# Kernel tuning notes

Hardware: AMD Instinct MI355X
Metric: run time of the kernel (lower is better)

## Reference

```python
import jax, jax.numpy as jnp
import numpy as np

B, IN, N, E = 2048, 1024, 64, 128
NEG_SLOPE = 0.01  # torch LeakyReLU default

def setup_inputs() -> dict:
    key = jax.random.key(0)
    k = jax.random.split(key, 5)
    scale_in = 1.0 / np.sqrt(IN)
    scale_ctx = 1.0 / np.sqrt(2 * E)
    return {
        "x": jax.random.normal(k[0], (B, IN), dtype=jnp.float32),
        # stacked per-concept Linear(in_features, 2*emb_size)
        "W_ctx": jax.random.uniform(k[1], (N, IN, 2 * E), jnp.float32, -scale_in, scale_in),
        "b_ctx": jax.random.uniform(k[2], (N, 2 * E), jnp.float32, -scale_in, scale_in),
        # shared Linear(2*emb_size, 1)
        "w_prob": jax.random.uniform(k[3], (2 * E,), jnp.float32, -scale_ctx, scale_ctx),
        "b_prob": jax.random.uniform(k[4], (), jnp.float32, -scale_ctx, scale_ctx),
    }

def reference(x, W_ctx, b_ctx, w_prob, b_prob):
    # context: [B, N, 2E] = LeakyReLU(x @ W_i + b_i) for all concepts i at once
    ctx = jnp.einsum("bi,nio->bno", x, W_ctx) + b_ctx
    ctx = jnp.where(ctx >= 0, ctx, NEG_SLOPE * ctx)
    # shared gate: [B, N]
    c_pred = jax.nn.sigmoid(jnp.einsum("bno,o->bn", ctx, w_prob) + b_prob)
    # gated blend of positive/negative halves -> [B, N, E]
    p = c_pred[..., None]
    c_emb = ctx[..., :E] * p + ctx[..., E:] * (1.0 - p)
    return c_emb, c_pred
```

## Files before the change

kernel.cpp:

```cpp
#include <hip/hip_runtime.h>
#include <hip/hip_bf16.h>

typedef __attribute__((ext_vector_type(4))) short short4v;
typedef __attribute__((ext_vector_type(8))) short short8v;
typedef __attribute__((ext_vector_type(4))) float floatx4;

#define B_ROWS 2048
#define K_DIM  1024
#define N_CON  64
#define TWO_E  256
#define E_DIM  128
#define BM     128
#define BK     64
#define NT     16
#define LDSA_BYTES (BM * BK * 2)
#define LDSB_BYTES (TWO_E * BK * 2)
#define TILE_BYTES (LDSA_BYTES + LDSB_BYTES)
#define NBUF 3
#define SMEM_DYN (TILE_BYTES * NBUF)
#define EMB_ELEMS 16777216ULL
#define WT_BYTES  33554432ULL
#define XB_BYTES  4194304ULL

static __device__ inline unsigned short bf16bits(float f) {
    __hip_bfloat16 h = __float2bfloat16(f);
    unsigned short u;
    __builtin_memcpy(&u, &h, 2);
    return u;
}

static __device__ inline void dma16(const void* g, void* l) {
    __builtin_amdgcn_global_load_lds(
        (const __attribute__((address_space(1))) unsigned int*)g,
        (__attribute__((address_space(3))) unsigned int*)l,
        16, 0, 0);
}

__global__ void __launch_bounds__(256) prep(const float* __restrict__ W,
                                            const float* __restrict__ x,
                                            unsigned short* __restrict__ Wt,
                                            unsigned short* __restrict__ xb) {
    __shared__ unsigned int lds2[64 * 36];
    const int tid = threadIdx.x;
    const int ot = blockIdx.x, ktile = blockIdx.y, n = blockIdx.z;
    const float* src = W + ((size_t)n * K_DIM + (size_t)ktile * 64) * TWO_E + ot * 64;
    unsigned short* dst = Wt + ((size_t)n * TWO_E + (size_t)ot * 64) * K_DIM + ktile * 64;

    const int kp = tid >> 4;
    const int c  = (tid & 15) * 4;
#pragma unroll
    for (int it = 0; it < 2; ++it) {
        const int k0 = it * 32 + kp * 2;
        floatx4 r0 = *(const floatx4*)&src[(size_t)k0 * TWO_E + c];
        floatx4 r1 = *(const floatx4*)&src[(size_t)(k0 + 1) * TWO_E + c];
#pragma unroll
        for (int j = 0; j < 4; ++j) {
            unsigned int d = (unsigned int)bf16bits(r0[j]) |
                             ((unsigned int)bf16bits(r1[j]) << 16);
            lds2[(c + j) * 36 + it * 16 + kp] = d;
        }
    }
    __syncthreads();
#pragma unroll
    for (int it = 0; it < 2; ++it) {
        int q = it * 256 + tid;
        int o = q >> 3, kc = q & 7;
        short8v v = *(short8v*)&lds2[o * 36 + kc * 4];
        *(short8v*)&dst[(size_t)o * K_DIM + kc * 8] = v;
    }

    const int bid = blockIdx.x + blockIdx.y * 4 + blockIdx.z * 64;
    const size_t base = (size_t)bid * 512 + (size_t)tid * 2;
    unsigned int d = (unsigned int)bf16bits(x[base]) |
                     ((unsigned int)bf16bits(x[base + 1]) << 16);
    ((unsigned int*)xb)[base >> 1] = d;
}

static __device__ inline void stage_A(const unsigned short* xrow, int kt,
                                      char* ldsA, int wave, int lane) {
#pragma unroll
    for (int it = 0; it < 2; ++it) {
        int c = it * 8 + wave;
        int s = c * 64 + lane;
        int r = s >> 3, g = s & 7;
        dma16(xrow + (size_t)r * K_DIM + kt + ((g ^ (r & 7)) * 8), ldsA + c * 1024);
    }
}

template <int I0, int I1>
static __device__ inline void stage_B(const unsigned short* wbase, int kt,
                                      char* ldsB, int wave, int lane) {
#pragma unroll
    for (int it = I0; it < I1; ++it) {
        int c = it * 8 + wave;
        int s = c * 64 + lane;
        int r = s >> 3, g = s & 7;
        dma16(wbase + (size_t)r * K_DIM + kt + ((g ^ (r & 7)) * 8), ldsB + c * 1024);
    }
}

__global__ void __launch_bounds__(512, 2)
concept_pipe(const unsigned short* __restrict__ xb,
             const unsigned short* __restrict__ Wt,
             const float* __restrict__ bc,
             const float* __restrict__ wp,
             const float* __restrict__ bp,
             float* __restrict__ out) {
    extern __shared__ __align__(16) char smem[];

    const int tid  = threadIdx.x;
    const int wave = tid >> 6;
    const int lane = tid & 63;
    const int lg   = lane >> 4;
    const int l15  = lane & 15;
    const int h    = wave >> 2;
    const int og   = wave & 3;

    const int lin = blockIdx.y * 16 + blockIdx.x;
    const int nid = (lin & 7) * 128 + (lin >> 3);
    const int rb  = nid & 15;
    const int n   = nid >> 4;

    int otile[4];
#pragma unroll
    for (int oi = 0; oi < 4; ++oi) otile[oi] = og * 32 + (oi & 1) * 16 + (oi & 2) * 64;

    floatx4 acc[4][4];
#pragma unroll
    for (int mi = 0; mi < 4; ++mi)
#pragma unroll
        for (int oi = 0; oi < 4; ++oi) acc[mi][oi] = (floatx4){0.f, 0.f, 0.f, 0.f};

    const unsigned short* xrow  = xb + (size_t)rb * BM * K_DIM;
    const unsigned short* wbase = Wt + (size_t)n * TWO_E * K_DIM;

    stage_A(xrow, 0, smem, wave, lane);
    stage_B<0, 4>(wbase, 0, smem + LDSA_BYTES, wave, lane);
    stage_A(xrow, BK, smem + TILE_BYTES, wave, lane);
    stage_B<0, 4>(wbase, BK, smem + TILE_BYTES + LDSA_BYTES, wave, lane);

    asm volatile("s_waitcnt vmcnt(6)" ::: "memory");
    __builtin_amdgcn_s_barrier();

    int cur = 0;
#pragma unroll 1
    for (int t = 0; t < NT; ++t) {
        char* ldsA = smem + cur * TILE_BYTES;
        char* ldsB = ldsA + LDSA_BYTES;
        int stg = cur + 2; if (stg >= NBUF) stg -= NBUF;
        char* stgA = smem + stg * TILE_BYTES;
        char* stgB = stgA + LDSA_BYTES;
        const int ktn = (t + 2) * BK;

        short8v af[4], bfr[4];

        {
            const int sw = (lg ^ (l15 & 7)) * 16;
#pragma unroll
            for (int mi = 0; mi < 4; ++mi)
                af[mi] = *(const short8v*)(ldsA + (h * 64 + mi * 16 + l15) * 128 + sw);
#pragma unroll
            for (int oi = 0; oi < 4; ++oi)
                bfr[oi] = *(const short8v*)(ldsB + (otile[oi] + l15) * 128 + sw);
        }
        if (t <= NT - 3) {
            stage_A(xrow, ktn, stgA, wave, lane);
            stage_B<0, 1>(wbase, ktn, stgB, wave, lane);
        }
        __builtin_amdgcn_s_barrier();
        asm volatile("s_waitcnt lgkmcnt(0)" ::: "memory");
        __builtin_amdgcn_sched_barrier(0);
        __builtin_amdgcn_s_setprio(1);
#pragma unroll
        for (int mi = 0; mi < 4; ++mi)
#pragma unroll
            for (int oi = 0; oi < 4; ++oi)
                acc[mi][oi] = __builtin_amdgcn_mfma_f32_16x16x32_bf16(
                    af[mi], bfr[oi], acc[mi][oi], 0, 0, 0);
        __builtin_amdgcn_s_setprio(0);
        __builtin_amdgcn_s_barrier();

        {
            const int sw = ((4 + lg) ^ (l15 & 7)) * 16;
#pragma unroll
            for (int mi = 0; mi < 4; ++mi)
                af[mi] = *(const short8v*)(ldsA + (h * 64 + mi * 16 + l15) * 128 + sw);
#pragma unroll
            for (int oi = 0; oi < 4; ++oi)
                bfr[oi] = *(const short8v*)(ldsB + (otile[oi] + l15) * 128 + sw);
        }
        if (t <= NT - 3)
            stage_B<1, 4>(wbase, ktn, stgB, wave, lane);
        __builtin_amdgcn_s_barrier();
        asm volatile("s_waitcnt lgkmcnt(0)" ::: "memory");
        __builtin_amdgcn_sched_barrier(0);
        __builtin_amdgcn_s_setprio(1);
#pragma unroll
        for (int mi = 0; mi < 4; ++mi)
#pragma unroll
            for (int oi = 0; oi < 4; ++oi)
                acc[mi][oi] = __builtin_amdgcn_mfma_f32_16x16x32_bf16(
                    af[mi], bfr[oi], acc[mi][oi], 0, 0, 0);
        __builtin_amdgcn_s_setprio(0);

        if (t <= NT - 3)      asm volatile("s_waitcnt vmcnt(6)" ::: "memory");
        else if (t == NT - 2) asm volatile("s_waitcnt vmcnt(0)" ::: "memory");
        if (t < NT - 1) __builtin_amdgcn_s_barrier();

        ++cur; if (cur == NBUF) cur = 0;
    }

    __syncthreads();

    float biasf[4], wpf[4];
#pragma unroll
    for (int oi = 0; oi < 4; ++oi) {
        int o = otile[oi] + l15;
        biasf[oi] = bc[n * TWO_E + o];
        wpf[oi]  = wp[o];
    }
#pragma unroll
    for (int mi = 0; mi < 4; ++mi)
#pragma unroll
        for (int oi = 0; oi < 4; ++oi)
#pragma unroll
            for (int j = 0; j < 4; ++j) {
                float v = acc[mi][oi][j] + biasf[oi];
                acc[mi][oi][j] = v >= 0.f ? v : 0.01f * v;
            }

    float* partial = (float*)smem;
    float* pv      = (float*)(smem + 2048);

#pragma unroll
    for (int mi = 0; mi < 4; ++mi)
#pragma unroll
        for (int j = 0; j < 4; ++j) {
            float ps = 0.f;
#pragma unroll
            for (int oi = 0; oi < 4; ++oi) ps += acc[mi][oi][j] * wpf[oi];
            ps += __shfl_xor(ps, 1);
            ps += __shfl_xor(ps, 2);
            ps += __shfl_xor(ps, 4);
            ps += __shfl_xor(ps, 8);
            if (l15 == 0) partial[(h * 64 + mi * 16 + lg * 4 + j) * 4 + og] = ps;
        }
    __syncthreads();

    if (tid < 128) {
        float s = partial[tid * 4] + partial[tid * 4 + 1] + partial[tid * 4 + 2] +
                  partial[tid * 4 + 3] + bp[0];
        float p = 1.f / (1.f + __expf(-s));
        pv[tid] = p;
        size_t bi = (size_t)rb * BM + tid;
        out[EMB_ELEMS + bi * N_CON + n] = p;
    }
    __syncthreads();

#pragma unroll
    for (int mi = 0; mi < 4; ++mi)
#pragma unroll
        for (int oi = 0; oi < 2; ++oi)
#pragma unroll
            for (int j = 0; j < 4; ++j) {
                int row = h * 64 + mi * 16 + lg * 4 + j;
                int e = og * 32 + oi * 16 + l15;
                float p = pv[row];
                float v = acc[mi][oi][j] * p + acc[mi][oi + 2][j] * (1.f - p);
                size_t bi = (size_t)rb * BM + row;
                out[(bi * N_CON + n) * E_DIM + e] = v;
            }
}

__global__ void __launch_bounds__(512, 4)
concept_fallback(const float* __restrict__ x,
                 const float* __restrict__ Wc,
                 const float* __restrict__ bc,
                 const float* __restrict__ wp,
                 const float* __restrict__ bp,
                 float* __restrict__ out) {
    __shared__ __align__(16) char smem[TILE_BYTES];
    char* ldsA = smem;
    char* ldsB = smem + LDSA_BYTES;

    const int tid  = threadIdx.x;
    const int wave = tid >> 6;
    const int lane = tid & 63;
    const int lg   = lane >> 4;
    const int l15  = lane & 15;
    const int h    = wave >> 2;
    const int og   = wave & 3;
    const int rb = blockIdx.x;
    const int n  = blockIdx.y;

    int otile[4];
#pragma unroll
    for (int oi = 0; oi < 4; ++oi) otile[oi] = og * 32 + (oi & 1) * 16 + (oi & 2) * 64;

    floatx4 acc[4][4];
#pragma unroll
    for (int mi = 0; mi < 4; ++mi)
#pragma unroll
        for (int oi = 0; oi < 4; ++oi) acc[mi][oi] = (floatx4){0.f, 0.f, 0.f, 0.f};

    const float* xg = x + (size_t)rb * BM * K_DIM;
    const float* wg = Wc + (size_t)n * K_DIM * TWO_E;

    for (int kt = 0; kt < K_DIM; kt += BK) {
#pragma unroll
        for (int it = 0; it < 2; ++it) {
            int s = it * 512 + tid;
            int r = s >> 3, g = s & 7;
            const float* p = xg + (size_t)r * K_DIM + kt + ((g ^ (r & 7)) * 8);
            floatx4 v0 = *(const floatx4*)p, v1 = *(const floatx4*)(p + 4);
            short8v b;
            b[0] = (short)bf16bits(v0[0]); b[1] = (short)bf16bits(v0[1]);
            b[2] = (short)bf16bits(v0[2]); b[3] = (short)bf16bits(v0[3]);
            b[4] = (short)bf16bits(v1[0]); b[5] = (short)bf16bits(v1[1]);
            b[6] = (short)bf16bits(v1[2]); b[7] = (short)bf16bits(v1[3]);
            *(short8v*)(ldsA + s * 16) = b;
        }
#pragma unroll
        for (int it = 0; it < 4; ++it) {
            int s = it * 512 + tid;
            int r = s >> 3, g = s & 7;
            int k0 = kt + (g ^ (r & 7)) * 8;
            short8v b;
#pragma unroll
            for (int j = 0; j < 8; ++j)
                b[j] = (short)bf16bits(wg[(size_t)(k0 + j) * TWO_E + r]);
            *(short8v*)(ldsB + s * 16) = b;
        }
        __syncthreads();

#pragma unroll
        for (int ks = 0; ks < 2; ++ks) {
            const int sw = ((ks * 4 + lg) ^ (l15 & 7)) * 16;
            short8v af[4], bfr[4];
#pragma unroll
            for (int mi = 0; mi < 4; ++mi)
                af[mi] = *(const short8v*)(ldsA + (h * 64 + mi * 16 + l15) * 128 + sw);
#pragma unroll
            for (int oi = 0; oi < 4; ++oi)
                bfr[oi] = *(const short8v*)(ldsB + (otile[oi] + l15) * 128 + sw);
#pragma unroll
            for (int mi = 0; mi < 4; ++mi)
#pragma unroll
                for (int oi = 0; oi < 4; ++oi)
                    acc[mi][oi] = __builtin_amdgcn_mfma_f32_16x16x32_bf16(
                        af[mi], bfr[oi], acc[mi][oi], 0, 0, 0);
        }
        __syncthreads();
    }

    float biasf[4], wpf[4];
#pragma unroll
    for (int oi = 0; oi < 4; ++oi) {
        int o = otile[oi] + l15;
        biasf[oi] = bc[n * TWO_E + o];
        wpf[oi]  = wp[o];
    }
#pragma unroll
    for (int mi = 0; mi < 4; ++mi)
#pragma unroll
        for (int oi = 0; oi < 4; ++oi)
#pragma unroll
            for (int j = 0; j < 4; ++j) {
                float v = acc[mi][oi][j] + biasf[oi];
                acc[mi][oi][j] = v >= 0.f ? v : 0.01f * v;
            }

    float* partial = (float*)smem;
    float* pv      = (float*)(smem + 2048);

#pragma unroll
    for (int mi = 0; mi < 4; ++mi)
#pragma unroll
        for (int j = 0; j < 4; ++j) {
            float ps = 0.f;
#pragma unroll
            for (int oi = 0; oi < 4; ++oi) ps += acc[mi][oi][j] * wpf[oi];
            ps += __shfl_xor(ps, 1);
            ps += __shfl_xor(ps, 2);
            ps += __shfl_xor(ps, 4);
            ps += __shfl_xor(ps, 8);
            if (l15 == 0) partial[(h * 64 + mi * 16 + lg * 4 + j) * 4 + og] = ps;
        }
    __syncthreads();

    if (tid < 128) {
        float s = partial[tid * 4] + partial[tid * 4 + 1] + partial[tid * 4 + 2] +
                  partial[tid * 4 + 3] + bp[0];
        float p = 1.f / (1.f + __expf(-s));
        pv[tid] = p;
        size_t bi = (size_t)rb * BM + tid;
        out[EMB_ELEMS + bi * N_CON + n] = p;
    }
    __syncthreads();

#pragma unroll
    for (int mi = 0; mi < 4; ++mi)
#pragma unroll
        for (int oi = 0; oi < 2; ++oi)
#pragma unroll
            for (int j = 0; j < 4; ++j) {
                int row = h * 64 + mi * 16 + lg * 4 + j;
                int e = og * 32 + oi * 16 + l15;
                float p = pv[row];
                float v = acc[mi][oi][j] * p + acc[mi][oi + 2][j] * (1.f - p);
                size_t bi = (size_t)rb * BM + row;
                out[(bi * N_CON + n) * E_DIM + e] = v;
            }
}

extern "C" void kernel_launch(void* const* d_in, const int* in_sizes, int n_in,
                              void* d_out, int out_size, void* d_ws, size_t ws_size,
                              hipStream_t stream) {
    const float* x  = (const float*)d_in[0];
    const float* Wc = (const float*)d_in[1];
    const float* bc = (const float*)d_in[2];
    const float* wp = (const float*)d_in[3];
    const float* bp = (const float*)d_in[4];
    float* out = (float*)d_out;

    if (ws_size >= WT_BYTES + XB_BYTES) {
        static bool s_attr_done = false;
        if (!s_attr_done) {
            hipFuncSetAttribute((const void*)concept_pipe,
                                hipFuncAttributeMaxDynamicSharedMemorySize,
                                SMEM_DYN);
            s_attr_done = true;
        }
        unsigned short* Wt = (unsigned short*)d_ws;
        unsigned short* xb = (unsigned short*)((char*)d_ws + WT_BYTES);
        prep<<<dim3(4, 16, 64), 256, 0, stream>>>(Wc, x, Wt, xb);
        concept_pipe<<<dim3(16, 64), 512, SMEM_DYN, stream>>>(
            xb, Wt, bc, wp, bp, out);
    } else {
        concept_fallback<<<dim3(16, 64), 512, 0, stream>>>(
            x, Wc, bc, wp, bp, out);
    }
}
```

Baseline: 206.8 us.

## Double row tile to 256 with double-buffered four-phase MFMA pipeline

Raises the per-block batch tile from 128 to 256 rows, so each wave keeps a 128x64 accumulator (8x4 fragments) and each staged W tile is reused across twice as many rows. The triple-buffer LDS pipeline becomes a double buffer whose next-tile DMA loads are split across four compute phases, and the grid is halved to 8x64 blocks. The aim is to halve the global/L2 traffic for weights and raise MFMA work per LDS load. The cost is higher register pressure under launch_bounds(512,2), fewer blocks to fill the GPU, and in-place buffer overwrites that rely on the barrier ordering being correct.

After: 198.1 us. -4.2%, faster.

```diff
diff --git a/kernel.cpp b/kernel.cpp
--- a/kernel.cpp
+++ b/kernel.cpp
@@ -10,14 +10,13 @@
 #define N_CON  64
 #define TWO_E  256
 #define E_DIM  128
-#define BM     128
+#define BM     256
 #define BK     64
 #define NT     16
 #define LDSA_BYTES (BM * BK * 2)
 #define LDSB_BYTES (TWO_E * BK * 2)
 #define TILE_BYTES (LDSA_BYTES + LDSB_BYTES)
-#define NBUF 3
-#define SMEM_DYN (TILE_BYTES * NBUF)
+#define SMEM_DYN (TILE_BYTES * 2)
 #define EMB_ELEMS 16777216ULL
 #define WT_BYTES  33554432ULL
 #define XB_BYTES  4194304ULL
@@ -76,36 +75,22 @@
     ((unsigned int*)xb)[base >> 1] = d;
 }
 
-static __device__ inline void stage_A(const unsigned short* xrow, int kt,
-                                      char* ldsA, int wave, int lane) {
-#pragma unroll
-    for (int it = 0; it < 2; ++it) {
-        int c = it * 8 + wave;
-        int s = c * 64 + lane;
-        int r = s >> 3, g = s & 7;
-        dma16(xrow + (size_t)r * K_DIM + kt + ((g ^ (r & 7)) * 8), ldsA + c * 1024);
-    }
-}
-
-template <int I0, int I1>
-static __device__ inline void stage_B(const unsigned short* wbase, int kt,
-                                      char* ldsB, int wave, int lane) {
-#pragma unroll
-    for (int it = I0; it < I1; ++it) {
-        int c = it * 8 + wave;
-        int s = c * 64 + lane;
-        int r = s >> 3, g = s & 7;
-        dma16(wbase + (size_t)r * K_DIM + kt + ((g ^ (r & 7)) * 8), ldsB + c * 1024);
-    }
+template <int IT>
+static __device__ inline void stA(const unsigned short* base, int kt,
+                                  char* lds, int wave, int lane) {
+    int c = IT * 8 + wave;
+    int s = c * 64 + lane;
+    int r = s >> 3, g = s & 7;
+    dma16(base + (size_t)r * K_DIM + kt + ((g ^ (r & 7)) * 8), lds + c * 1024);
 }
 
 __global__ void __launch_bounds__(512, 2)
-concept_pipe(const unsigned short* __restrict__ xb,
-             const unsigned short* __restrict__ Wt,
-             const float* __restrict__ bc,
-             const float* __restrict__ wp,
-             const float* __restrict__ bp,
-             float* __restrict__ out) {
+concept_256(const unsigned short* __restrict__ xb,
+            const unsigned short* __restrict__ Wt,
+            const float* __restrict__ bc,
+            const float* __restrict__ wp,
+            const float* __restrict__ bp,
+            float* __restrict__ out) {
     extern __shared__ __align__(16) char smem[];
 
     const int tid  = threadIdx.x;
@@ -116,57 +101,62 @@
     const int h    = wave >> 2;
     const int og   = wave & 3;
 
-    const int lin = blockIdx.y * 16 + blockIdx.x;
-    const int nid = (lin & 7) * 128 + (lin >> 3);
-    const int rb  = nid & 15;
-    const int n   = nid >> 4;
+    const int lin = blockIdx.y * 8 + blockIdx.x;
+    const int nid = (lin & 7) * 64 + (lin >> 3);
+    const int rb  = nid & 7;
+    const int n   = nid >> 3;
 
     int otile[4];
 #pragma unroll
     for (int oi = 0; oi < 4; ++oi) otile[oi] = og * 32 + (oi & 1) * 16 + (oi & 2) * 64;
 
-    floatx4 acc[4][4];
-#pragma unroll
-    for (int mi = 0; mi < 4; ++mi)
+    floatx4 acc[8][4];
+#pragma unroll
+    for (int mi = 0; mi < 8; ++mi)
 #pragma unroll
         for (int oi = 0; oi < 4; ++oi) acc[mi][oi] = (floatx4){0.f, 0.f, 0.f, 0.f};
 
     const unsigned short* xrow  = xb + (size_t)rb * BM * K_DIM;
     const unsigned short* wbase = Wt + (size_t)n * TWO_E * K_DIM;
 
-    stage_A(xrow, 0, smem, wave, lane);
-    stage_B<0, 4>(wbase, 0, smem + LDSA_BYTES, wave, lane);
-    stage_A(xrow, BK, smem + TILE_BYTES, wave, lane);
-    stage_B<0, 4>(wbase, BK, smem + TILE_BYTES + LDSA_BYTES, wave, lane);
-
-    asm volatile("s_waitcnt vmcnt(6)" ::: "memory");
+    char* bufA0 = smem;
+    char* bufB0 = smem + LDSA_BYTES;
+    char* bufA1 = smem + TILE_BYTES;
+    char* bufB1 = bufA1 + LDSA_BYTES;
+
+    stA<0>(xrow, 0, bufA0, wave, lane);  stA<1>(xrow, 0, bufA0, wave, lane);
+    stA<2>(xrow, 0, bufA0, wave, lane);  stA<3>(xrow, 0, bufA0, wave, lane);
+    stA<0>(wbase, 0, bufB0, wave, lane); stA<1>(wbase, 0, bufB0, wave, lane);
+    stA<2>(wbase, 0, bufB0, wave, lane); stA<3>(wbase, 0, bufB0, wave, lane);
+    stA<0>(xrow, BK, bufA1, wave, lane);  stA<1>(xrow, BK, bufA1, wave, lane);
+    stA<2>(xrow, BK, bufA1, wave, lane);  stA<3>(xrow, BK, bufA1, wave, lane);
+    stA<0>(wbase, BK, bufB1, wave, lane); stA<1>(wbase, BK, bufB1, wave, lane);
+    stA<2>(wbase, BK, bufB1, wave, lane); stA<3>(wbase, BK, bufB1, wave, lane);
+
+    asm volatile("s_waitcnt vmcnt(8)" ::: "memory");
     __builtin_amdgcn_s_barrier();
 
-    int cur = 0;
+    const int arow0 = h * 128;
+    short8v af[4][2], bf[2][2], bf2[2][2];
+
 #pragma unroll 1
     for (int t = 0; t < NT; ++t) {
-        char* ldsA = smem + cur * TILE_BYTES;
+        char* ldsA = smem + (t & 1) * TILE_BYTES;
         char* ldsB = ldsA + LDSA_BYTES;
-        int stg = cur + 2; if (stg >= NBUF) stg -= NBUF;
-        char* stgA = smem + stg * TILE_BYTES;
-        char* stgB = stgA + LDSA_BYTES;
+        const bool stg = (t + 2 < NT);
         const int ktn = (t + 2) * BK;
 
-        short8v af[4], bfr[4];
-
-        {
-            const int sw = (lg ^ (l15 & 7)) * 16;
+#pragma unroll
+        for (int ks = 0; ks < 2; ++ks) {
+            const int sw = ((ks * 4 + lg) ^ (l15 & 7)) * 16;
 #pragma unroll
             for (int mi = 0; mi < 4; ++mi)
-                af[mi] = *(const short8v*)(ldsA + (h * 64 + mi * 16 + l15) * 128 + sw);
-#pragma unroll
-            for (int oi = 0; oi < 4; ++oi)
-                bfr[oi] = *(const short8v*)(ldsB + (otile[oi] + l15) * 128 + sw);
-        }
-        if (t <= NT - 3) {
-            stage_A(xrow, ktn, stgA, wave, lane);
-            stage_B<0, 1>(wbase, ktn, stgB, wave, lane);
-        }
+                af[mi][ks] = *(const short8v*)(ldsA + (arow0 + mi * 16 + l15) * 128 + sw);
+#pragma unroll
+            for (int oi = 0; oi < 2; ++oi)
+                bf[oi][ks] = *(const short8v*)(ldsB + (otile[oi] + l15) * 128 + sw);
+        }
+        asm volatile("s_waitcnt lgkmcnt(8)" ::: "memory");
         __builtin_amdgcn_s_barrier();
         asm volatile("s_waitcnt lgkmcnt(0)" ::: "memory");
         __builtin_amdgcn_sched_barrier(0);
@@ -174,23 +164,27 @@
 #pragma unroll
         for (int mi = 0; mi < 4; ++mi)
 #pragma unroll
-            for (int oi = 0; oi < 4; ++oi)
-                acc[mi][oi] = __builtin_amdgcn_mfma_f32_16x16x32_bf16(
-                    af[mi], bfr[oi], acc[mi][oi], 0, 0, 0);
+            for (int oi = 0; oi < 2; ++oi)
+#pragma unroll
+                for (int ks = 0; ks < 2; ++ks)
+                    acc[mi][oi] = __builtin_amdgcn_mfma_f32_16x16x32_bf16(
+                        af[mi][ks], bf[oi][ks], acc[mi][oi], 0, 0, 0);
         __builtin_amdgcn_s_setprio(0);
         __builtin_amdgcn_s_barrier();
 
-        {
-            const int sw = ((4 + lg) ^ (l15 & 7)) * 16;
-#pragma unroll
-            for (int mi = 0; mi < 4; ++mi)
-                af[mi] = *(const short8v*)(ldsA + (h * 64 + mi * 16 + l15) * 128 + sw);
-#pragma unroll
-            for (int oi = 0; oi < 4; ++oi)
-                bfr[oi] = *(const short8v*)(ldsB + (otile[oi] + l15) * 128 + sw);
-        }
-        if (t <= NT - 3)
-            stage_B<1, 4>(wbase, ktn, stgB, wave, lane);
+#pragma unroll
+        for (int ks = 0; ks < 2; ++ks) {
+            const int sw = ((ks * 4 + lg) ^ (l15 & 7)) * 16;
+#pragma unroll
+            for (int oi = 0; oi < 2; ++oi)
+                bf2[oi][ks] = *(const short8v*)(ldsB + (otile[2 + oi] + l15) * 128 + sw);
+        }
+        if (stg) {
+            stA<0>(xrow, ktn, ldsA, wave, lane);
+            stA<2>(xrow, ktn, ldsA, wave, lane);
+            stA<0>(wbase, ktn, ldsB, wave, lane);
+            stA<1>(wbase, ktn, ldsB, wave, lane);
+        }
         __builtin_amdgcn_s_barrier();
         asm volatile("s_waitcnt lgkmcnt(0)" ::: "memory");
         __builtin_amdgcn_sched_barrier(0);
@@ -198,19 +192,59 @@
 #pragma unroll
         for (int mi = 0; mi < 4; ++mi)
 #pragma unroll
-            for (int oi = 0; oi < 4; ++oi)
-                acc[mi][oi] = __builtin_amdgcn_mfma_f32_16x16x32_bf16(
-                    af[mi], bfr[oi], acc[mi][oi], 0, 0, 0);
+            for (int oi = 0; oi < 2; ++oi)
+#pragma unroll
+                for (int ks = 0; ks < 2; ++ks)
+                    acc[mi][2 + oi] = __builtin_amdgcn_mfma_f32_16x16x32_bf16(
+                        af[mi][ks], bf2[oi][ks], acc[mi][2 + oi], 0, 0, 0);
         __builtin_amdgcn_s_setprio(0);
-
-        if (t <= NT - 3)      asm volatile("s_waitcnt vmcnt(6)" ::: "memory");
-        else if (t == NT - 2) asm volatile("s_waitcnt vmcnt(0)" ::: "memory");
-        if (t < NT - 1) __builtin_amdgcn_s_barrier();
-
-        ++cur; if (cur == NBUF) cur = 0;
-    }
-
-    __syncthreads();
+        __builtin_amdgcn_s_barrier();
+
+#pragma unroll
+        for (int ks = 0; ks < 2; ++ks) {
+            const int sw = ((ks * 4 + lg) ^ (l15 & 7)) * 16;
+#pragma unroll
+            for (int mi = 0; mi < 4; ++mi)
+                af[mi][ks] = *(const short8v*)(ldsA + (arow0 + 64 + mi * 16 + l15) * 128 + sw);
+        }
+        if (stg) {
+            stA<2>(wbase, ktn, ldsB, wave, lane);
+            stA<3>(wbase, ktn, ldsB, wave, lane);
+        }
+        __builtin_amdgcn_s_barrier();
+        asm volatile("s_waitcnt lgkmcnt(0)" ::: "memory");
+        __builtin_amdgcn_sched_barrier(0);
+        __builtin_amdgcn_s_setprio(1);
+#pragma unroll
+        for (int mi = 0; mi < 4; ++mi)
+#pragma unroll
+            for (int oi = 0; oi < 2; ++oi)
+#pragma unroll
+                for (int ks = 0; ks < 2; ++ks)
+                    acc[4 + mi][2 + oi] = __builtin_amdgcn_mfma_f32_16x16x32_bf16(
+                        af[mi][ks], bf2[oi][ks], acc[4 + mi][2 + oi], 0, 0, 0);
+        __builtin_amdgcn_s_setprio(0);
+        __builtin_amdgcn_s_barrier();
+
+        if (stg) {
+            stA<1>(xrow, ktn, ldsA, wave, lane);
+            stA<3>(xrow, ktn, ldsA, wave, lane);
+        }
+        __builtin_amdgcn_s_setprio(1);
+#pragma unroll
+        for (int mi = 0; mi < 4; ++mi)
+#pragma unroll
+            for (int oi = 0; oi < 2; ++oi)
+#pragma unroll
+                for (int ks = 0; ks < 2; ++ks)
+                    acc[4 + mi][oi] = __builtin_amdgcn_mfma_f32_16x16x32_bf16(
+                        af[mi][ks], bf[oi][ks], acc[4 + mi][oi], 0, 0, 0);
+        __builtin_amdgcn_s_setprio(0);
+
+        if (stg) asm volatile("s_waitcnt vmcnt(8)" ::: "memory");
+        else     asm volatile("s_waitcnt vmcnt(0)" ::: "memory");
+        __builtin_amdgcn_s_barrier();
+    }
 
     float biasf[4], wpf[4];
 #pragma unroll
@@ -220,7 +254,7 @@
         wpf[oi]  = wp[o];
     }
 #pragma unroll
-    for (int mi = 0; mi < 4; ++mi)
+    for (int mi = 0; mi < 8; ++mi)
 #pragma unroll
         for (int oi = 0; oi < 4; ++oi)
 #pragma unroll
@@ -230,10 +264,10 @@
             }
 
     float* partial = (float*)smem;
-    float* pv      = (float*)(smem + 2048);
-
-#pragma unroll
-    for (int mi = 0; mi < 4; ++mi)
+    float* pv      = (float*)(smem + 4096);
+
+#pragma unroll
+    for (int mi = 0; mi < 8; ++mi)
 #pragma unroll
         for (int j = 0; j < 4; ++j) {
             float ps = 0.f;
@@ -243,11 +277,11 @@
             ps += __shfl_xor(ps, 2);
             ps += __shfl_xor(ps, 4);
             ps += __shfl_xor(ps, 8);
-            if (l15 == 0) partial[(h * 64 + mi * 16 + lg * 4 + j) * 4 + og] = ps;
+            if (l15 == 0) partial[(h * 128 + mi * 16 + lg * 4 + j) * 4 + og] = ps;
         }
     __syncthreads();
 
-    if (tid < 128) {
+    if (tid < 256) {
         float s = partial[tid * 4] + partial[tid * 4 + 1] + partial[tid * 4 + 2] +
                   partial[tid * 4 + 3] + bp[0];
         float p = 1.f / (1.f + __expf(-s));
@@ -258,12 +292,12 @@
     __syncthreads();
 
 #pragma unroll
-    for (int mi = 0; mi < 4; ++mi)
+    for (int mi = 0; mi < 8; ++mi)
 #pragma unroll
         for (int oi = 0; oi < 2; ++oi)
 #pragma unroll
             for (int j = 0; j < 4; ++j) {
-                int row = h * 64 + mi * 16 + lg * 4 + j;
+                int row = h * 128 + mi * 16 + lg * 4 + j;
                 int e = og * 32 + oi * 16 + l15;
                 float p = pv[row];
                 float v = acc[mi][oi][j] * p + acc[mi][oi + 2][j] * (1.f - p);
@@ -279,9 +313,9 @@
                  const float* __restrict__ wp,
                  const float* __restrict__ bp,
                  float* __restrict__ out) {
-    __shared__ __align__(16) char smem[TILE_BYTES];
+    __shared__ __align__(16) char smem[49152];
     char* ldsA = smem;
-    char* ldsB = smem + LDSA_BYTES;
+    char* ldsB = smem + 16384;
 
     const int tid  = threadIdx.x;
     const int wave = tid >> 6;
@@ -303,7 +337,7 @@
 #pragma unroll
         for (int oi = 0; oi < 4; ++oi) acc[mi][oi] = (floatx4){0.f, 0.f, 0.f, 0.f};
 
-    const float* xg = x + (size_t)rb * BM * K_DIM;
+    const float* xg = x + (size_t)rb * 128 * K_DIM;
     const float* wg = Wc + (size_t)n * K_DIM * TWO_E;
 
     for (int kt = 0; kt < K_DIM; kt += BK) {
@@ -393,7 +427,7 @@
                   partial[tid * 4 + 3] + bp[0];
         float p = 1.f / (1.f + __expf(-s));
         pv[tid] = p;
-        size_t bi = (size_t)rb * BM + tid;
+        size_t bi = (size_t)rb * 128 + tid;
         out[EMB_ELEMS + bi * N_CON + n] = p;
     }
     __syncthreads();
@@ -408,7 +442,7 @@
                 int e = og * 32 + oi * 16 + l15;
                 float p = pv[row];
                 float v = acc[mi][oi][j] * p + acc[mi][oi + 2][j] * (1.f - p);
-                size_t bi = (size_t)rb * BM + row;
+                size_t bi = (size_t)rb * 128 + row;
                 out[(bi * N_CON + n) * E_DIM + e] = v;
             }
 }
@@ -426,7 +460,7 @@
     if (ws_size >= WT_BYTES + XB_BYTES) {
         static bool s_attr_done = false;
         if (!s_attr_done) {
-            hipFuncSetAttribute((const void*)concept_pipe,
+            hipFuncSetAttribute((const void*)concept_256,
                                 hipFuncAttributeMaxDynamicSharedMemorySize,
                                 SMEM_DYN);
             s_attr_done = true;
@@ -434,7 +468,7 @@
         unsigned short* Wt = (unsigned short*)d_ws;
         unsigned short* xb = (unsigned short*)((char*)d_ws + WT_BYTES);
         prep<<<dim3(4, 16, 64), 256, 0, stream>>>(Wc, x, Wt, xb);
-        concept_pipe<<<dim3(16, 64), 512, SMEM_DYN, stream>>>(
+        concept_256<<<dim3(8, 64), 512, SMEM_DYN, stream>>>(
             xb, Wt, bc, wp, bp, out);
     } else {
         concept_fallback<<<dim3(16, 64), 512, 0, stream>>>(
```
